# Performance work log

Measured on AMD Instinct MI355X. Metric: run time of the kernel, lower is better.

Reference implementation:

```python
import jax, jax.numpy as jnp
import numpy as np

B, F, V, E = 65536, 39, 100000, 16
EPS = 1e-5

def setup_inputs() -> dict:
    key = jax.random.key(0)
    ks = jax.random.split(key, 10)
    return {
        'Xi': jax.random.randint(ks[0], (B, F, 1), 0, V, dtype=jnp.int64) if jax.config.read('jax_enable_x64') else jax.random.randint(ks[0], (B, F, 1), 0, V, dtype=jnp.int32),
        'Xv': jax.random.uniform(ks[1], (B, F), dtype=jnp.float32),
        'emb1': jax.random.normal(ks[2], (F, V, 1), dtype=jnp.float32),
        'emb2': jax.random.normal(ks[3], (F, V, E), dtype=jnp.float32),
        'W1': jax.random.normal(ks[4], (F * E, 512), dtype=jnp.float32) * 0.02,
        'b1': jax.random.normal(ks[5], (512,), dtype=jnp.float32) * 0.02,
        'g1': jnp.ones((512,), jnp.float32),
        'be1': jnp.zeros((512,), jnp.float32),
        'W2': jax.random.normal(ks[6], (512, 256), dtype=jnp.float32) * 0.02,
        'b2': jax.random.normal(ks[7], (256,), dtype=jnp.float32) * 0.02,
        'g2': jnp.ones((256,), jnp.float32),
        'be2': jnp.zeros((256,), jnp.float32),
        'bias': jax.random.normal(ks[8], (1,), dtype=jnp.float32),
    }

def _batchnorm(x, g, b):
    mu = jnp.mean(x, axis=0)
    var = jnp.mean(jnp.square(x - mu), axis=0)  # biased var, torch BN training mode
    return (x - mu) * jax.lax.rsqrt(var + EPS) * g + b

def reference(Xi, Xv, emb1, emb2, W1, b1, g1, be1, W2, b2, g2, be2, bias):
    idx = Xi[:, :, 0]                                # [B, F]
    fidx = jnp.arange(F)[None, :]                    # [1, F]
    # fused per-field gathers: [B, F] and [B, F, E]
    first = emb1[fidx, idx, 0] * Xv                  # first-order, [B, F]
    fm2 = emb2[fidx, idx] * Xv[:, :, None]           # second-order embeds, [B, F, E]
    sum_emb = jnp.sum(fm2, axis=1)                   # [B, E]
    second = 0.5 * (jnp.square(sum_emb) - jnp.sum(jnp.square(fm2), axis=1))  # [B, E]
    # deep part (note: original forward never applies the final num_classes layer)
    deep = fm2.reshape(B, F * E)
    deep = _batchnorm(deep @ W1 + b1, g1, be1)
    deep = _batchnorm(deep @ W2 + b2, g2, be2)
    return bias + jnp.sum(first, axis=1) + jnp.sum(second, axis=1) + jnp.sum(deep, axis=1)
```

## Files before the change

kernel.cpp:

```cpp
#include <hip/hip_runtime.h>

#define B_ROWS 65536
#define F_FEAT 39
#define V_VOC  100000
#define D_PAD  640
#define BN_EPS 1e-5f

typedef __bf16 bf16x8 __attribute__((ext_vector_type(8)));
typedef float  f32x16 __attribute__((ext_vector_type(16)));

__device__ __forceinline__ unsigned short toBF(float x) {
  unsigned int u = __float_as_uint(x);
  u += 0x7fffu + ((u >> 16) & 1u);
  return (unsigned short)(u >> 16);
}

__global__ __launch_bounds__(256) void k1_gather(
    const int* __restrict__ Xi, const float* __restrict__ Xv,
    const float* __restrict__ emb1, const float* __restrict__ emb2,
    unsigned short* __restrict__ XT, float* __restrict__ fs,
    float* __restrict__ Mz) {
  if (threadIdx.x < 100)
    Mz[(size_t)blockIdx.x * 100 + threadIdx.x] = 0.f;

  const int b0 = blockIdx.x * 16;
  __shared__ int            sIdx[16][40];
  __shared__ float          sXv[16][40];
  __shared__ unsigned short xt[16][648];

  for (int u = threadIdx.x; u < 16 * 39; u += 256) {
    int r = u / 39, f = u - r * 39;
    sIdx[r][f] = Xi[(size_t)(b0 + r) * 39 + f];
    sXv[r][f]  = Xv[(size_t)(b0 + r) * 39 + f];
  }
  __syncthreads();

  const int r = threadIdx.x >> 4, ec = threadIdx.x & 15;
  float sv = 0.f, ss = 0.f;
#pragma unroll 4
  for (int f = 0; f < 39; ++f) {
    int id = sIdx[r][f];
    float xv = sXv[r][f];
    float a = emb2[((size_t)f * V_VOC + id) * 16 + ec] * xv;
    sv += a; ss += a * a;
    xt[r][f * 16 + ec] = toBF(a);
  }
  float fo = 0.f;
  for (int f = ec; f < 39; f += 16)
    fo += emb1[(size_t)f * V_VOC + sIdx[r][f]] * sXv[r][f];

  float q = 0.5f * (sv * sv - ss) + fo;
  q += __shfl_xor(q, 1);
  q += __shfl_xor(q, 2);
  q += __shfl_xor(q, 4);
  q += __shfl_xor(q, 8);
  if (ec == 0) fs[b0 + r] = q;
  __syncthreads();

  for (int m = threadIdx.x; m < 640; m += 256) {
    unsigned short* dst = XT + (size_t)m * B_ROWS + b0;
    unsigned int q2[8];
    if (m < 624) {
#pragma unroll
      for (int rr = 0; rr < 8; ++rr)
        q2[rr] = (unsigned int)xt[2 * rr][m] | ((unsigned int)xt[2 * rr + 1][m] << 16);
    } else {
      unsigned int fill = (m == 624) ? 0x3f803f80u : 0u;
#pragma unroll
      for (int rr = 0; rr < 8; ++rr) q2[rr] = fill;
    }
    uint4 w0, w1;
    w0.x = q2[0]; w0.y = q2[1]; w0.z = q2[2]; w0.w = q2[3];
    w1.x = q2[4]; w1.y = q2[5]; w1.z = q2[6]; w1.w = q2[7];
    *reinterpret_cast<uint4*>(dst)     = w0;
    *reinterpret_cast<uint4*>(dst + 8) = w1;
  }
}

#define KSPLIT 32
__global__ __launch_bounds__(256) void k2_syrk(const unsigned short* __restrict__ XT,
                                               float* __restrict__ M) {
  const int ks = blockIdx.x & (KSPLIT - 1);
  int pair = blockIdx.x >> 5;
  int ti = 0, p = pair;
  while (p >= 5 - ti) { p -= 5 - ti; ++ti; }
  const int tj = ti + p;

  __shared__ unsigned short pa[128 * 64];
  __shared__ unsigned short pb[128 * 64];

  const int lane = threadIdx.x & 63, wid = threadIdx.x >> 6;
  const int wm = wid >> 1, wn = wid & 1;
  const int rl = lane & 31, hh = lane >> 5;

  f32x16 acc00, acc01, acc10, acc11;
#pragma unroll
  for (int i = 0; i < 16; ++i) { acc00[i] = 0.f; acc01[i] = 0.f; acc10[i] = 0.f; acc11[i] = 0.f; }

  const int krange = B_ROWS / KSPLIT;
  const int kbase = ks * krange;

  for (int kt = 0; kt < krange; kt += 64) {
    const int k0 = kbase + kt;
#pragma unroll
    for (int g2 = 0; g2 < 4; ++g2) {
      const int g = threadIdx.x + g2 * 256;
      const int r = g >> 3, j = g & 7;
      uint4 va = *reinterpret_cast<const uint4*>(XT + (size_t)(ti * 128 + r) * B_ROWS + k0 + j * 8);
      *reinterpret_cast<uint4*>((char*)pa + r * 128 + ((j ^ (r & 7)) << 4)) = va;
      uint4 vb = *reinterpret_cast<const uint4*>(XT + (size_t)(tj * 128 + r) * B_ROWS + k0 + j * 8);
      *reinterpret_cast<uint4*>((char*)pb + r * 128 + ((j ^ (r & 7)) << 4)) = vb;
    }
    __syncthreads();
#pragma unroll
    for (int kc = 0; kc < 4; ++kc) {
      const int ra0 = wm * 64 + rl, ra1 = wm * 64 + 32 + rl;
      const int rb0 = wn * 64 + rl, rb1 = wn * 64 + 32 + rl;
      bf16x8 a0 = *reinterpret_cast<const bf16x8*>((char*)pa + ra0 * 128 + (((kc * 2 + hh) ^ (ra0 & 7)) << 4));
      bf16x8 a1 = *reinterpret_cast<const bf16x8*>((char*)pa + ra1 * 128 + (((kc * 2 + hh) ^ (ra1 & 7)) << 4));
      bf16x8 b0 = *reinterpret_cast<const bf16x8*>((char*)pb + rb0 * 128 + (((kc * 2 + hh) ^ (rb0 & 7)) << 4));
      bf16x8 b1 = *reinterpret_cast<const bf16x8*>((char*)pb + rb1 * 128 + (((kc * 2 + hh) ^ (rb1 & 7)) << 4));
      acc00 = __builtin_amdgcn_mfma_f32_32x32x16_bf16(a0, b0, acc00, 0, 0, 0);
      acc01 = __builtin_amdgcn_mfma_f32_32x32x16_bf16(a0, b1, acc01, 0, 0, 0);
      acc10 = __builtin_amdgcn_mfma_f32_32x32x16_bf16(a1, b0, acc10, 0, 0, 0);
      acc11 = __builtin_amdgcn_mfma_f32_32x32x16_bf16(a1, b1, acc11, 0, 0, 0);
    }
    __syncthreads();
  }

#pragma unroll
  for (int rr = 0; rr < 16; ++rr) {
    const int rloc = (rr & 3) + ((rr >> 2) << 3) + hh * 4;
    const int row0 = ti * 128 + wm * 64 + rloc;
    const int row1 = row0 + 32;
    const int col0 = tj * 128 + wn * 64 + rl;
    atomicAdd(&M[row0 * D_PAD + col0], acc00[rr]);
    atomicAdd(&M[row0 * D_PAD + col0 + 32], acc01[rr]);
    atomicAdd(&M[row1 * D_PAD + col0], acc10[rr]);
    atomicAdd(&M[row1 * D_PAD + col0 + 32], acc11[rr]);
  }
}

__device__ __forceinline__ float fetchM(const float* M, int a, int b) {
  if ((a >> 7) > (b >> 7)) { int t = a; a = b; b = t; }
  return M[a * D_PAD + b];
}
__global__ void k3a_cov(const float* __restrict__ M, float* __restrict__ Cov,
                        float* __restrict__ mu) {
  const int i = blockIdx.x;
  const float inv = 1.f / 65536.f;
  const float mui = fetchM(M, 624, i) * inv;
  for (int j = threadIdx.x; j < D_PAD; j += 256) {
    float muj = fetchM(M, 624, j) * inv;
    Cov[i * D_PAD + j] = fetchM(M, i, j) * inv - mui * muj;
    if (i == 0) mu[j] = muj;
  }
}

__global__ __launch_bounds__(256) void qform(const float* __restrict__ Cov,
                                             const float* __restrict__ W, const int ldw,
                                             const float* __restrict__ g,
                                             float* __restrict__ alpha) {
  const int k0 = blockIdx.x * 2;
  __shared__ float w0s[624], w1s[624];
  for (int i = threadIdx.x; i < 624; i += 256) {
    w0s[i] = W[(size_t)i * ldw + k0];
    w1s[i] = W[(size_t)i * ldw + k0 + 1];
  }
  __syncthreads();
  const int j0 = threadIdx.x, j1 = threadIdx.x + 256, j2 = threadIdx.x + 512;
  const bool v2 = (j2 < 624);
  const float wj00 = w0s[j0], wj01 = w0s[j1], wj02 = v2 ? w0s[j2] : 0.f;
  const float wj10 = w1s[j0], wj11 = w1s[j1], wj12 = v2 ? w1s[j2] : 0.f;
  float acc0 = 0.f, acc1 = 0.f;
  for (int i = 0; i < 624; ++i) {
    const float wi0 = w0s[i], wi1 = w1s[i];
    const float* row = Cov + i * D_PAD;
    const float c0 = row[j0], c1 = row[j1], c2 = v2 ? row[j2] : 0.f;
    acc0 += wi0 * (c0 * wj00 + c1 * wj01 + c2 * wj02);
    acc1 += wi1 * (c0 * wj10 + c1 * wj11 + c2 * wj12);
  }
#pragma unroll
  for (int off = 32; off > 0; off >>= 1) {
    acc0 += __shfl_down(acc0, off);
    acc1 += __shfl_down(acc1, off);
  }
  __shared__ float pr[2][4];
  const int lane = threadIdx.x & 63, wv = threadIdx.x >> 6;
  if (lane == 0) { pr[0][wv] = acc0; pr[1][wv] = acc1; }
  __syncthreads();
  if (threadIdx.x == 0) {
    float v0 = pr[0][0] + pr[0][1] + pr[0][2] + pr[0][3];
    float v1 = pr[1][0] + pr[1][1] + pr[1][2] + pr[1][3];
    alpha[k0]     = g[k0]     * rsqrtf(v0 + BN_EPS);
    alpha[k0 + 1] = g[k0 + 1] * rsqrtf(v1 + BN_EPS);
  }
}

__global__ __launch_bounds__(256) void k3c_G(const float* __restrict__ W1,
                                             const float* __restrict__ alpha1,
                                             const float* __restrict__ W2,
                                             float* __restrict__ G) {
  const int i = blockIdx.x;
  __shared__ float a[512];
  for (int k = threadIdx.x; k < 512; k += 256)
    a[k] = W1[(size_t)i * 512 + k] * alpha1[k];
  __syncthreads();
  const int j = threadIdx.x;
  float acc = 0.f;
#pragma unroll 8
  for (int k = 0; k < 512; ++k) acc += a[k] * W2[(size_t)k * 256 + j];
  G[(size_t)i * 256 + j] = acc;
}

__global__ __launch_bounds__(256) void k3e_final(const float* __restrict__ G,
                                                 const float* __restrict__ alpha2,
                                                 const float* __restrict__ mu,
                                                 const float* __restrict__ be2,
                                                 const float* __restrict__ bias,
                                                 float* __restrict__ gw,
                                                 float* __restrict__ consts) {
  __shared__ float a2[256];
  __shared__ float gws[640];
  a2[threadIdx.x] = alpha2[threadIdx.x];
  __syncthreads();
  for (int i = threadIdx.x; i < 640; i += 256) {
    float acc = 0.f;
    if (i < 624) {
      const float* gr = G + (size_t)i * 256;
#pragma unroll 8
      for (int j = 0; j < 256; ++j) acc += gr[j] * a2[j];
    }
    gw[i] = acc;
    gws[i] = acc;
  }
  __syncthreads();
  float pm = 0.f;
  for (int i = threadIdx.x; i < 624; i += 256) pm += mu[i] * gws[i];
  float val = be2[threadIdx.x] - pm;
#pragma unroll
  for (int off = 32; off > 0; off >>= 1) val += __shfl_down(val, off);
  __shared__ float pr[4];
  const int lane = threadIdx.x & 63, wv = threadIdx.x >> 6;
  if (lane == 0) pr[wv] = val;
  __syncthreads();
  if (threadIdx.x == 0) consts[0] = bias[0] + pr[0] + pr[1] + pr[2] + pr[3];
}

__global__ __launch_bounds__(256) void k5_dot(const unsigned short* __restrict__ XT,
                                              const float* __restrict__ gw,
                                              const float* __restrict__ fs,
                                              const float* __restrict__ consts,
                                              float* __restrict__ out) {
  __shared__ float g[624];
  for (int m = threadIdx.x; m < 624; m += 256) g[m] = gw[m];
  __syncthreads();
  const int b = blockIdx.x * 256 + threadIdx.x;
  const unsigned short* col = XT + b;
  float acc = 0.f;
#pragma unroll 8
  for (int m = 0; m < 624; ++m) {
    unsigned int u = (unsigned int)col[(size_t)m * B_ROWS] << 16;
    acc += __uint_as_float(u) * g[m];
  }
  out[b] = acc + fs[b] + consts[0];
}

extern "C" void kernel_launch(void* const* d_in, const int* in_sizes, int n_in,
                              void* d_out, int out_size, void* d_ws, size_t ws_size,
                              hipStream_t stream) {
  const int*   Xi   = (const int*)d_in[0];
  const float* Xv   = (const float*)d_in[1];
  const float* emb1 = (const float*)d_in[2];
  const float* emb2 = (const float*)d_in[3];
  const float* W1   = (const float*)d_in[4];
  const float* g1   = (const float*)d_in[6];
  const float* W2   = (const float*)d_in[8];
  const float* g2   = (const float*)d_in[10];
  const float* be2  = (const float*)d_in[11];
  const float* bias = (const float*)d_in[12];
  float* out = (float*)d_out;
  char* ws = (char*)d_ws;

  const size_t OFF_XT  = 0;
  const size_t OFF_M   = OFF_XT + (size_t)640 * 65536 * 2;
  const size_t OFF_COV = OFF_M + (size_t)640 * 640 * 4;
  const size_t OFF_MU  = OFF_COV + (size_t)640 * 640 * 4;
  const size_t OFF_A1  = OFF_MU + 640 * 4;
  const size_t OFF_A2  = OFF_A1 + 512 * 4;
  const size_t OFF_G   = OFF_A2 + 256 * 4;
  const size_t OFF_GW  = OFF_G + (size_t)624 * 256 * 4;
  const size_t OFF_CN  = OFF_GW + 640 * 4;
  const size_t OFF_FS  = OFF_CN + 256;

  unsigned short* XT = (unsigned short*)(ws + OFF_XT);
  float* M   = (float*)(ws + OFF_M);
  float* COV = (float*)(ws + OFF_COV);
  float* MU  = (float*)(ws + OFF_MU);
  float* A1  = (float*)(ws + OFF_A1);
  float* A2  = (float*)(ws + OFF_A2);
  float* G   = (float*)(ws + OFF_G);
  float* GW  = (float*)(ws + OFF_GW);
  float* CN  = (float*)(ws + OFF_CN);
  float* FS  = (float*)(ws + OFF_FS);

  k1_gather<<<4096, 256, 0, stream>>>(Xi, Xv, emb1, emb2, XT, FS, M);
  k2_syrk<<<15 * KSPLIT, 256, 0, stream>>>(XT, M);
  k3a_cov<<<640, 256, 0, stream>>>(M, COV, MU);
  qform<<<256, 256, 0, stream>>>(COV, W1, 512, g1, A1);
  k3c_G<<<624, 256, 0, stream>>>(W1, A1, W2, G);
  qform<<<128, 256, 0, stream>>>(COV, G, 256, g2, A2);
  k3e_final<<<1, 256, 0, stream>>>(G, A2, MU, be2, bias, GW, CN);
  k5_dot<<<256, 256, 0, stream>>>(XT, GW, FS, CN, out);
}
```

Baseline: 400.6 us.

## Vectorize emb2 gather with float4 loads and move first-order term to final kernel

```diff
diff --git a/kernel.cpp b/kernel.cpp
--- a/kernel.cpp
+++ b/kernel.cpp
@@ -17,7 +17,7 @@
 
 __global__ __launch_bounds__(256) void k1_gather(
     const int* __restrict__ Xi, const float* __restrict__ Xv,
-    const float* __restrict__ emb1, const float* __restrict__ emb2,
+    const float* __restrict__ emb2,
     unsigned short* __restrict__ XT, float* __restrict__ fs,
     float* __restrict__ Mz) {
   if (threadIdx.x < 100)
@@ -35,26 +35,42 @@
   }
   __syncthreads();
 
-  const int r = threadIdx.x >> 4, ec = threadIdx.x & 15;
-  float sv = 0.f, ss = 0.f;
-#pragma unroll 4
-  for (int f = 0; f < 39; ++f) {
-    int id = sIdx[r][f];
-    float xv = sXv[r][f];
-    float a = emb2[((size_t)f * V_VOC + id) * 16 + ec] * xv;
-    sv += a; ss += a * a;
-    xt[r][f * 16 + ec] = toBF(a);
-  }
-  float fo = 0.f;
-  for (int f = ec; f < 39; f += 16)
-    fo += emb1[(size_t)f * V_VOC + sIdx[r][f]] * sXv[r][f];
-
-  float q = 0.5f * (sv * sv - ss) + fo;
-  q += __shfl_xor(q, 1);
-  q += __shfl_xor(q, 2);
-  q += __shfl_xor(q, 4);
-  q += __shfl_xor(q, 8);
-  if (ec == 0) fs[b0 + r] = q;
+  const int r   = threadIdx.x >> 4;
+  const int l16 = threadIdx.x & 15;
+  const int seg = l16 & 3;
+  const int fo  = l16 >> 2;
+
+  float4 sv = {0.f, 0.f, 0.f, 0.f};
+  float  ss = 0.f;
+#pragma unroll
+  for (int it = 0; it < 10; ++it) {
+    const int f = it * 4 + fo;
+    if (f < 39) {
+      const int   id = sIdx[r][f];
+      const float xv = sXv[r][f];
+      const float4 v = *reinterpret_cast<const float4*>(
+          emb2 + ((size_t)f * V_VOC + id) * 16 + seg * 4);
+      const float a0 = v.x * xv, a1 = v.y * xv, a2 = v.z * xv, a3 = v.w * xv;
+      sv.x += a0; sv.y += a1; sv.z += a2; sv.w += a3;
+      ss += a0 * a0 + a1 * a1 + a2 * a2 + a3 * a3;
+      uint2 pk;
+      pk.x = (unsigned int)toBF(a0) | ((unsigned int)toBF(a1) << 16);
+      pk.y = (unsigned int)toBF(a2) | ((unsigned int)toBF(a3) << 16);
+      *reinterpret_cast<uint2*>(&xt[r][f * 16 + seg * 4]) = pk;
+    }
+  }
+  sv.x += __shfl_xor(sv.x, 4); sv.y += __shfl_xor(sv.y, 4);
+  sv.z += __shfl_xor(sv.z, 4); sv.w += __shfl_xor(sv.w, 4);
+  sv.x += __shfl_xor(sv.x, 8); sv.y += __shfl_xor(sv.y, 8);
+  sv.z += __shfl_xor(sv.z, 8); sv.w += __shfl_xor(sv.w, 8);
+  float s2 = sv.x * sv.x + sv.y * sv.y + sv.z * sv.z + sv.w * sv.w;
+  s2 += __shfl_xor(s2, 1);
+  s2 += __shfl_xor(s2, 2);
+  ss += __shfl_xor(ss, 1);
+  ss += __shfl_xor(ss, 2);
+  ss += __shfl_xor(ss, 4);
+  ss += __shfl_xor(ss, 8);
+  if (l16 == 0) fs[b0 + r] = 0.5f * (s2 - ss);
   __syncthreads();
 
   for (int m = threadIdx.x; m < 640; m += 256) {
@@ -247,23 +263,40 @@
   if (threadIdx.x == 0) consts[0] = bias[0] + pr[0] + pr[1] + pr[2] + pr[3];
 }
 
-__global__ __launch_bounds__(256) void k5_dot(const unsigned short* __restrict__ XT,
+__global__ __launch_bounds__(256) void k5_out(const int* __restrict__ Xi,
+                                              const float* __restrict__ Xv,
+                                              const float* __restrict__ emb1,
+                                              const unsigned short* __restrict__ XT,
                                               const float* __restrict__ gw,
                                               const float* __restrict__ fs,
                                               const float* __restrict__ consts,
                                               float* __restrict__ out) {
+  const int b0 = blockIdx.x * 128;
+  __shared__ int   si[128][40];
+  __shared__ float sx[128][40];
   __shared__ float g[624];
   for (int m = threadIdx.x; m < 624; m += 256) g[m] = gw[m];
-  __syncthreads();
-  const int b = blockIdx.x * 256 + threadIdx.x;
+  for (int u = threadIdx.x; u < 128 * 39; u += 256) {
+    int rr = u / 39, ff = u - rr * 39;
+    si[rr][ff] = Xi[(size_t)b0 * 39 + u];
+    sx[rr][ff] = Xv[(size_t)b0 * 39 + u];
+  }
+  __syncthreads();
+  const int r = threadIdx.x >> 1, h = threadIdx.x & 1;
+  const int b = b0 + r;
+  float acc = 0.f;
   const unsigned short* col = XT + b;
-  float acc = 0.f;
+  const int m0 = h * 312;
 #pragma unroll 8
-  for (int m = 0; m < 624; ++m) {
+  for (int m = m0; m < m0 + 312; ++m) {
     unsigned int u = (unsigned int)col[(size_t)m * B_ROWS] << 16;
     acc += __uint_as_float(u) * g[m];
   }
-  out[b] = acc + fs[b] + consts[0];
+  const int fb = h ? 20 : 0, fe = h ? 39 : 20;
+  for (int f = fb; f < fe; ++f)
+    acc += emb1[(size_t)f * V_VOC + si[r][f]] * sx[r][f];
+  acc += __shfl_xor(acc, 1);
+  if (h == 0) out[b] = acc + fs[b] + consts[0];
 }
 
 extern "C" void kernel_launch(void* const* d_in, const int* in_sizes, int n_in,
@@ -304,12 +337,12 @@
   float* CN  = (float*)(ws + OFF_CN);
   float* FS  = (float*)(ws + OFF_FS);
 
-  k1_gather<<<4096, 256, 0, stream>>>(Xi, Xv, emb1, emb2, XT, FS, M);
+  k1_gather<<<4096, 256, 0, stream>>>(Xi, Xv, emb2, XT, FS, M);
   k2_syrk<<<15 * KSPLIT, 256, 0, stream>>>(XT, M);
   k3a_cov<<<640, 256, 0, stream>>>(M, COV, MU);
   qform<<<256, 256, 0, stream>>>(COV, W1, 512, g1, A1);
   k3c_G<<<624, 256, 0, stream>>>(W1, A1, W2, G);
   qform<<<128, 256, 0, stream>>>(COV, G, 256, g2, A2);
   k3e_final<<<1, 256, 0, stream>>>(G, A2, MU, be2, bias, GW, CN);
-  k5_dot<<<256, 256, 0, stream>>>(XT, GW, FS, CN, out);
-}
+  k5_out<<<512, 256, 0, stream>>>(Xi, Xv, emb1, XT, GW, FS, CN, out);
+}
```

Result: faster. 360.4 us (-10.0%).
